# Kernel tuning notes

Hardware: AMD Instinct MI355X
Metric: run time of the kernel (lower is better)

## Reference

```python
import jax, jax.numpy as jnp
import numpy as np

B, S, IN, H = 64, 512, 64, 512


def _lin_init(key, fan_in, fan_out):
    k1, k2 = jax.random.split(key)
    bound = 1.0 / np.sqrt(fan_in)
    W = jax.random.uniform(k1, (fan_in, fan_out), jnp.float32, -bound, bound)
    b = jax.random.uniform(k2, (fan_out,), jnp.float32, -bound, bound)
    return W, b


def setup_inputs() -> dict:
    key = jax.random.key(0)
    ks = jax.random.split(key, 5)
    x = jax.random.normal(ks[0], (B, S, IN), jnp.float32)
    # Layer 0: 5 gates fused -> [IN+H, 5H]; layer 1 -> [H+H, 5H]
    W0, b0 = _lin_init(ks[1], IN + H, 5 * H)
    W1, b1 = _lin_init(ks[2], H + H, 5 * H)
    Wa, ba = _lin_init(ks[3], H, 1)
    Wfc, bfc = _lin_init(ks[4], H, 1)
    return {"x": x, "W0": W0, "b0": b0, "W1": W1, "b1": b1,
            "Wa": Wa, "ba": ba, "Wfc": Wfc, "bfc": bfc}


def _cell(xt, h, c, W, b):
    # one fused GEMM for the 5 gates (same math as 5 separate Linears)
    g = jnp.concatenate([xt, h], axis=-1) @ W + b  # [B, 5H]
    f, i, ch, o, e = jnp.split(g, 5, axis=-1)
    f = jax.nn.sigmoid(f)
    i = jax.nn.sigmoid(i)
    ch = jnp.tanh(ch)
    o = jax.nn.sigmoid(o)
    e = jax.nn.sigmoid(e)
    c_new = f * c + i * ch
    h_lin = o * jnp.tanh(c_new)
    h_new = e * jnp.exp(h_lin) + (1.0 - e) * h_lin  # exponential gating
    return h_new, c_new


def reference(x, W0, b0, W1, b1, Wa, ba, Wfc, bfc):
    Bx = x.shape[0]
    z = jnp.zeros((Bx, H), x.dtype)

    def step(carry, xt):
        (h0, c0), (h1, c1) = carry
        h0, c0 = _cell(xt, h0, c0, W0, b0)
        h1, c1 = _cell(h0, h1, c1, W1, b1)
        return ((h0, c0), (h1, c1)), h1

    _, hs = jax.lax.scan(step, ((z, z), (z, z)), jnp.swapaxes(x, 0, 1))
    lstm_out = jnp.swapaxes(hs, 0, 1)  # [B, S, H]
    att = jax.nn.softmax(lstm_out @ Wa + ba, axis=1)  # [B, S, 1], softmax over seq
    ctx = jnp.sum(att * lstm_out, axis=1)  # [B, H]
    out = ctx @ Wfc + bfc  # [B, 1]
    return out, att
```

## Files before the change

### kernel.cpp

```cpp
#include <hip/hip_runtime.h>
#include <hip/hip_cooperative_groups.h>
#include <math.h>

namespace cg = cooperative_groups;

#define BB 64
#define SS 512
#define INF 64
#define HH 512
#define G5 2560

typedef unsigned short u16;
typedef __attribute__((ext_vector_type(8))) short short8v;
typedef __attribute__((ext_vector_type(4))) float f32x4;

__global__ void init_kernel(float* __restrict__ p, int n) {
    int i = blockIdx.x * blockDim.x + threadIdx.x;
    if (i < n) p[i] = 0.f;
}

__device__ __forceinline__ void bf16_split(float f, u16& hi, u16& lo) {
    unsigned u = __float_as_uint(f);
    unsigned h = (u + 0x7FFFu + ((u >> 16) & 1u)) >> 16;
    float fh = __uint_as_float(h << 16);
    float r = f - fh;
    unsigned ur = __float_as_uint(r);
    unsigned l = (ur + 0x7FFFu + ((ur >> 16) & 1u)) >> 16;
    hi = (u16)h; lo = (u16)l;
}

__device__ __forceinline__ short8v ldfrag(const u16* p, int lane) {
    return *(const short8v*)(p + ((size_t)lane << 3));
}

__device__ __forceinline__ short8v llc_load(const u16* p, int lane) {
    short8v r;
    const u16* addr = p + ((size_t)lane << 3);
    asm volatile("global_load_dwordx4 %0, %1, off sc0 sc1"
                 : "=v"(r) : "v"(addr) : "memory");
    return r;
}

__global__ __launch_bounds__(256) void wrepack_frag(
    const float* __restrict__ W, u16* __restrict__ wf, int NS)
{
    const int s = blockIdx.x, J = blockIdx.y;
    const int tid = threadIdx.x;
    for (int v = tid; v < 2560; v += 256) {
        int g = v >> 9, rem = v & 511, kloc = rem >> 4, jloc = rem & 15;
        float w = W[(size_t)(s * 32 + kloc) * G5 + g * 512 + J * 16 + jloc];
        u16 hi, lo; bf16_split(w, hi, lo);
        int l = ((kloc >> 3) << 4) | jloc;
        size_t base = ((((size_t)J * 5 + g) * NS + s) * 2) * 512;
        size_t off = (size_t)l * 8 + (kloc & 7);
        wf[base + off] = hi;
        wf[base + 512 + off] = lo;
    }
}

__global__ __launch_bounds__(256) void xfrag_kernel(
    const float* __restrict__ x, u16* __restrict__ xf)
{
    const int t = blockIdx.x, tid = threadIdx.x;
    const size_t tb = (size_t)t * 2 * 4096;
    for (int rep = 0; rep < 4; ++rep) {
        int rrow = (tid >> 4) + rep * 16;
        int kq = (tid & 15) * 4;
        float4 v = *(const float4*)(x + ((size_t)rrow * SS + t) * INF + kq);
        float vals[4] = {v.x, v.y, v.z, v.w};
        #pragma unroll
        for (int c = 0; c < 4; ++c) {
            int k = kq + c;
            int sloc = k >> 5, kloc = k & 31;
            int m = rrow >> 4, rowloc = rrow & 15;
            int l = rowloc | ((kloc >> 3) << 4);
            size_t off = (size_t)sloc * 2048 + m * 512 + l * 8 + (kloc & 7);
            u16 hi, lo; bf16_split(vals[c], hi, lo);
            xf[tb + off] = hi;
            xf[tb + 4096 + off] = lo;
        }
    }
}

__device__ __forceinline__ void dom_arrive(unsigned* bar, int dom, int step) {
    unsigned r = __hip_atomic_fetch_add(bar + dom * 32, 1u,
                                        __ATOMIC_RELAXED, __HIP_MEMORY_SCOPE_AGENT);
    if (r == (unsigned)(step + 1) * 32u - 1u)
        __hip_atomic_store(bar + dom * 32 + 16, (unsigned)(step + 1),
                           __ATOMIC_RELAXED, __HIP_MEMORY_SCOPE_AGENT);
}
__device__ __forceinline__ void dom_wait(unsigned* bar, int dom, int val) {
    while ((int)__hip_atomic_load(bar + dom * 32 + 16,
                                  __ATOMIC_RELAXED, __HIP_MEMORY_SCOPE_AGENT) < val) {}
}

template<bool ISL1>
__device__ __forceinline__ void run_layer(
    const u16* __restrict__ xf, const u16* __restrict__ wf,
    u16* __restrict__ h0f, u16* __restrict__ h1f,
    const float* __restrict__ bv, float* __restrict__ lstm_out,
    unsigned* __restrict__ bar, float (*red)[5][64][4])
{
    constexpr int NS   = ISL1 ? 32 : 18;
    constexpr int MAXK = ISL1 ? 4 : 3;

    const int tid  = threadIdx.x;
    const int lane = tid & 63;
    const int wv   = tid >> 6;
    const int blk  = (int)blockIdx.x & 127;
    const int qq = blk >> 3, rr = blk & 7;
    const int J = rr * 4 + (qq & 3);
    const int m = qq >> 2;
    const int domSelf  = (ISL1 ? 4 : 0) + m;
    const int domOther = (ISL1 ? 0 : 4) + m;

    const int rowloc = (tid & 255) >> 4, jloc = tid & 15;
    const int row = m * 16 + rowloc;
    const int jg  = J * 16 + jloc;
    const int ltid = ((rowloc >> 2) << 4) | jloc;
    const int itid = rowloc & 3;

    float bias[5];
    #pragma unroll
    for (int g = 0; g < 5; ++g) bias[g] = bv[g * HH + jg];

    const int wkloc = ((J & 1) << 4) | jloc;
    const int wof = ((J >> 1) * 4 + m) * 512
                  + (rowloc | ((wkloc >> 3) << 4)) * 8 + (jloc & 7);

    short8v wH[MAXK][5], wL[MAXK][5];
    #pragma unroll
    for (int i = 0; i < MAXK; ++i) {
        const int s = wv + 8 * i;
        if (s < NS) {
            #pragma unroll
            for (int g = 0; g < 5; ++g) {
                const u16* wb = wf + ((((size_t)J * 5 + g) * NS + s) * 2) * 512;
                wH[i][g] = ldfrag(wb, lane);
                wL[i][g] = ldfrag(wb + 512, lane);
            }
        }
    }

    float c_reg = 0.f;
    float pend  = 0.f;

    for (int w = 0; w < SS; ++w) {
        if (tid == 0) {
            if (ISL1) {
                if (w >= 1) dom_wait(bar, domSelf, w);
                dom_wait(bar, domOther, w + 1);
            } else {
                if (w >= 1) dom_wait(bar, domSelf, w);
                if (w >= 4) dom_wait(bar, domOther, w - 3);
            }
        }
        __syncthreads();

        if (ISL1 && w >= 1 && tid < 256)
            lstm_out[((size_t)row * SS + (w - 1)) * HH + jg] = pend;

        short8v aH[MAXK], aL[MAXK];
        #pragma unroll
        for (int i = 0; i < MAXK; ++i) {
            const int s = wv + 8 * i;
            if (s < NS) {
                if (ISL1) {
                    const u16* p0;
                    const u16* p1;
                    if (s < 16) {
                        p0 = h0f + (size_t)((((w & 3) * 2 + 0) * 32768) + s * 2048 + m * 512);
                        p1 = h0f + (size_t)((((w & 3) * 2 + 1) * 32768) + s * 2048 + m * 512);
                    } else {
                        p0 = h1f + (size_t)(((((w + 1) & 1) * 2 + 0) * 32768) + (s - 16) * 2048 + m * 512);
                        p1 = h1f + (size_t)(((((w + 1) & 1) * 2 + 1) * 32768) + (s - 16) * 2048 + m * 512);
                    }
                    aH[i] = llc_load(p0, lane); aL[i] = llc_load(p1, lane);
                } else {
                    if (s < 2) {
                        const u16* p0 = xf + (size_t)((w * 2 + 0) * 4096 + s * 2048 + m * 512);
                        const u16* p1 = xf + (size_t)((w * 2 + 1) * 4096 + s * 2048 + m * 512);
                        aH[i] = ldfrag(p0, lane); aL[i] = ldfrag(p1, lane);
                    } else {
                        const u16* p0 = h0f + (size_t)(((((w + 3) & 3) * 2 + 0) * 32768) + (s - 2) * 2048 + m * 512);
                        const u16* p1 = h0f + (size_t)(((((w + 3) & 3) * 2 + 1) * 32768) + (s - 2) * 2048 + m * 512);
                        aH[i] = llc_load(p0, lane); aL[i] = llc_load(p1, lane);
                    }
                }
            }
        }

        asm volatile("s_waitcnt vmcnt(0)" ::: "memory");
        __builtin_amdgcn_sched_barrier(0);

        f32x4 acc[5];
        #pragma unroll
        for (int g = 0; g < 5; ++g) acc[g] = (f32x4){0.f, 0.f, 0.f, 0.f};

        #pragma unroll
        for (int i = 0; i < MAXK; ++i) {
            const int s = wv + 8 * i;
            if (s < NS) {
                #pragma unroll
                for (int g = 0; g < 5; ++g) {
                    acc[g] = __builtin_amdgcn_mfma_f32_16x16x32_bf16(aH[i], wH[i][g], acc[g], 0, 0, 0);
                    acc[g] = __builtin_amdgcn_mfma_f32_16x16x32_bf16(aH[i], wL[i][g], acc[g], 0, 0, 0);
                    acc[g] = __builtin_amdgcn_mfma_f32_16x16x32_bf16(aL[i], wH[i][g], acc[g], 0, 0, 0);
                }
            }
        }

        #pragma unroll
        for (int g = 0; g < 5; ++g)
            *(f32x4*)&red[wv][g][lane][0] = acc[g];
        __syncthreads();

        if (tid < 256) {
            float gv[5];
            #pragma unroll
            for (int g = 0; g < 5; ++g)
                gv[g] = ((red[0][g][ltid][itid] + red[1][g][ltid][itid])
                      +  (red[2][g][ltid][itid] + red[3][g][ltid][itid]))
                      + ((red[4][g][ltid][itid] + red[5][g][ltid][itid])
                      +  (red[6][g][ltid][itid] + red[7][g][ltid][itid]))
                      + bias[g];

            float f  = 1.f / (1.f + expf(-gv[0]));
            float i_ = 1.f / (1.f + expf(-gv[1]));
            float ch = tanhf(gv[2]);
            float o  = 1.f / (1.f + expf(-gv[3]));
            float e_ = 1.f / (1.f + expf(-gv[4]));

            c_reg = f * c_reg + i_ * ch;
            float hl = o * tanhf(c_reg);
            float hn = e_ * expf(hl) + (1.f - e_) * hl;

            u16 hi, lo; bf16_split(hn, hi, lo);
            if (ISL1) {
                const int par = w & 1;
                __hip_atomic_store(h1f + (size_t)((par * 2 + 0) * 32768) + wof, hi,
                                   __ATOMIC_RELAXED, __HIP_MEMORY_SCOPE_AGENT);
                __hip_atomic_store(h1f + (size_t)((par * 2 + 1) * 32768) + wof, lo,
                                   __ATOMIC_RELAXED, __HIP_MEMORY_SCOPE_AGENT);
                pend = hn;
            } else {
                const int par = w & 3;
                __hip_atomic_store(h0f + (size_t)((par * 2 + 0) * 32768) + wof, hi,
                                   __ATOMIC_RELAXED, __HIP_MEMORY_SCOPE_AGENT);
                __hip_atomic_store(h0f + (size_t)((par * 2 + 1) * 32768) + wof, lo,
                                   __ATOMIC_RELAXED, __HIP_MEMORY_SCOPE_AGENT);
            }
        }
        __syncthreads();
        if (tid == 0) dom_arrive(bar, domSelf, w);
    }
    if (ISL1 && threadIdx.x < 256)
        lstm_out[((size_t)row * SS + (SS - 1)) * HH + jg] = pend;
}

__global__ __launch_bounds__(512, 1) void persist_mfma(
    const u16* __restrict__ xf,
    const u16* __restrict__ wf0, const u16* __restrict__ wf1,
    const float* __restrict__ b0v, const float* __restrict__ b1v,
    u16* __restrict__ h0f, u16* __restrict__ h1f,
    float* __restrict__ lstm_out, unsigned* __restrict__ bar)
{
    __shared__ float red[8][5][64][4];
    if (blockIdx.x >= 128)
        run_layer<true >(xf, wf1, h0f, h1f, b1v, lstm_out, bar, red);
    else
        run_layer<false>(xf, wf0, h0f, h1f, b0v, lstm_out, bar, red);
}

__global__ __launch_bounds__(256) void repack_kernel(
    const float* __restrict__ W, float* __restrict__ P, int K)
{
    __shared__ float tile[64][65];
    const int tid = threadIdx.x;
    const int kt = blockIdx.x;
    const int c0 = blockIdx.y * 64;

    for (int e = tid; e < 64 * 16; e += 256) {
        int kr = e >> 4, cq = (e & 15) * 4;
        float4 v = *(const float4*)(W + (size_t)(kt * 64 + kr) * G5 + c0 + cq);
        tile[kr][cq + 0] = v.x; tile[kr][cq + 1] = v.y;
        tile[kr][cq + 2] = v.z; tile[kr][cq + 3] = v.w;
    }
    __syncthreads();

    const int gate = c0 >> 9;
    const int jb   = c0 & 511;
    for (int e = tid; e < 64 * 16; e += 256) {
        int lr = e >> 4;
        int kq = (e & 15) * 4;
        int j  = jb + lr;
        int g  = j >> 1;
        int c  = j & 1;
        int orow = g * 10 + gate * 2 + c;
        float4 v;
        v.x = tile[kq + 0][lr]; v.y = tile[kq + 1][lr];
        v.z = tile[kq + 2][lr]; v.w = tile[kq + 3][lr];
        *(float4*)(P + (size_t)orow * K + kt * 64 + kq) = v;
    }
}

__global__ __launch_bounds__(256) void xpose_kernel(
    const float* __restrict__ x, float* __restrict__ xT)
{
    __shared__ float tile[64][68];
    const int tid = threadIdx.x;
    const int t = blockIdx.x;

    for (int e = tid; e < 64 * 16; e += 256) {
        int row = e >> 4, kq = (e & 15) * 4;
        float4 v = *(const float4*)(x + ((size_t)row * SS + t) * INF + kq);
        tile[row][kq + 0] = v.x; tile[row][kq + 1] = v.y;
        tile[row][kq + 2] = v.z; tile[row][kq + 3] = v.w;
    }
    __syncthreads();
    float* dst = xT + (size_t)t * (INF * BB);
    for (int e = tid; e < INF * BB; e += 256) {
        int k = e >> 6, r = e & 63;
        dst[(k >> 2) * 256 + r * 4 + (k & 3)] = tile[r][k];
    }
}

__device__ __forceinline__ void gemm_seg(
    const float4* __restrict__ ap, const float4* __restrict__ wq,
    int K4, int nq, float* __restrict__ acc)
{
    #pragma unroll 2
    for (int q = 0; q < nq; ++q) {
        float4 a  = ap[q * 64];
        float4 w0 = wq[q + 0 * K4];
        float4 w1 = wq[q + 1 * K4];
        float4 w2 = wq[q + 2 * K4];
        float4 w3 = wq[q + 3 * K4];
        float4 w4 = wq[q + 4 * K4];
        float4 w5 = wq[q + 5 * K4];
        float4 w6 = wq[q + 6 * K4];
        float4 w7 = wq[q + 7 * K4];
        float4 w8 = wq[q + 8 * K4];
        float4 w9 = wq[q + 9 * K4];
        acc[0]=fmaf(a.x,w0.x,acc[0]); acc[0]=fmaf(a.y,w0.y,acc[0]);
        acc[0]=fmaf(a.z,w0.z,acc[0]); acc[0]=fmaf(a.w,w0.w,acc[0]);
        acc[1]=fmaf(a.x,w1.x,acc[1]); acc[1]=fmaf(a.y,w1.y,acc[1]);
        acc[1]=fmaf(a.z,w1.z,acc[1]); acc[1]=fmaf(a.w,w1.w,acc[1]);
        acc[2]=fmaf(a.x,w2.x,acc[2]); acc[2]=fmaf(a.y,w2.y,acc[2]);
        acc[2]=fmaf(a.z,w2.z,acc[2]); acc[2]=fmaf(a.w,w2.w,acc[2]);
        acc[3]=fmaf(a.x,w3.x,acc[3]); acc[3]=fmaf(a.y,w3.y,acc[3]);
        acc[3]=fmaf(a.z,w3.z,acc[3]); acc[3]=fmaf(a.w,w3.w,acc[3]);
        acc[4]=fmaf(a.x,w4.x,acc[4]); acc[4]=fmaf(a.y,w4.y,acc[4]);
        acc[4]=fmaf(a.z,w4.z,acc[4]); acc[4]=fmaf(a.w,w4.w,acc[4]);
        acc[5]=fmaf(a.x,w5.x,acc[5]); acc[5]=fmaf(a.y,w5.y,acc[5]);
        acc[5]=fmaf(a.z,w5.z,acc[5]); acc[5]=fmaf(a.w,w5.w,acc[5]);
        acc[6]=fmaf(a.x,w6.x,acc[6]); acc[6]=fmaf(a.y,w6.y,acc[6]);
        acc[6]=fmaf(a.z,w6.z,acc[6]); acc[6]=fmaf(a.w,w6.w,acc[6]);
        acc[7]=fmaf(a.x,w7.x,acc[7]); acc[7]=fmaf(a.y,w7.y,acc[7]);
        acc[7]=fmaf(a.z,w7.z,acc[7]); acc[7]=fmaf(a.w,w7.w,acc[7]);
        acc[8]=fmaf(a.x,w8.x,acc[8]); acc[8]=fmaf(a.y,w8.y,acc[8]);
        acc[8]=fmaf(a.z,w8.z,acc[8]); acc[8]=fmaf(a.w,w8.w,acc[8]);
        acc[9]=fmaf(a.x,w9.x,acc[9]); acc[9]=fmaf(a.y,w9.y,acc[9]);
        acc[9]=fmaf(a.z,w9.z,acc[9]); acc[9]=fmaf(a.w,w9.w,acc[9]);
    }
}

__global__ __launch_bounds__(256, 2) void step512_kernel(
    const float* __restrict__ xT,
    const float* __restrict__ P0, const float* __restrict__ b0v,
    const float* __restrict__ P1, const float* __restrict__ b1v,
    float* __restrict__ h0buf, float* __restrict__ h1buf,
    float* __restrict__ c0buf, float* __restrict__ c1buf,
    float* __restrict__ lstm_out, int t)
{
    __shared__ float W_s[10 * 1024];
    __shared__ float red[4][10][64];

    const int tid  = threadIdx.x;
    const int lane = tid & 63;
    const int wv   = tid >> 6;
    const bool isL1 = (blockIdx.x >= 256);
    const int blk  = (int)blockIdx.x & 255;
    const int g    = (blk & 7) * 32 + (blk >> 3);
    const int j    = g * 2 + (wv & 1);

    const bool active = isL1 ? (t >= 1) : (t < SS);
    if (!active) return;

    const int K  = isL1 ? 1024 : 576;
    const int K4 = K >> 2;
    const int QK = K >> 2;
    const int k0 = wv * QK;

    {
        const float* Pg = (isL1 ? P1 : P0) + (size_t)g * 10 * K;
        const int n4 = 10 * K / 4;
        for (int i = tid; i < n4; i += 256)
            *(float4*)&W_s[i * 4] = *(const float4*)(Pg + (size_t)i * 4);
    }
    __syncthreads();

    const int tm1 = t - 1;
    const float* h0prev = h0buf + ((t + 1) & 1) * (BB * HH);
    const float* h0cur  = h0buf + (tm1 & 1) * (BB * HH);
    const float* h1prev = h1buf + ((tm1 + 1) & 1) * (BB * HH);

    const float4* wq0 = (const float4*)W_s + (k0 >> 2);

    float acc[10];
    #pragma unroll
    for (int r = 0; r < 10; ++r) acc[r] = 0.f;

    if (!isL1) {
        if (wv == 0) {
            const float4* aX = (const float4*)(xT + (size_t)t * (INF * BB)) + lane;
            const float4* aH = (const float4*)h0prev + lane;
            gemm_seg(aX, wq0,      K4, 16, acc);
            gemm_seg(aH, wq0 + 16, K4, 20, acc);
        } else {
            const float4* aH = (const float4*)h0prev + (36 * wv - 16) * 64 + lane;
            gemm_seg(aH, wq0, K4, 36, acc);
        }
    } else {
        const float* src = (wv < 2) ? h0cur : h1prev;
        const float4* aH = (const float4*)src + (wv & 2 ? (wv - 2) : wv) * 4096 + lane;
        gemm_seg(aH, wq0, K4, 64, acc);
    }

    #pragma unroll
    for (int r = 0; r < 10; ++r) red[wv][r][lane] = acc[r];
    __syncthreads();

    if (wv < 2) {
        const float* bv = isL1 ? b1v : b0v;
        float gv[5];
        #pragma unroll
        for (int gate = 0; gate < 5; ++gate) {
            int r = gate * 2 + wv;
            gv[gate] = red[0][r][lane] + red[1][r][lane]
                     + red[2][r][lane] + red[3][r][lane] + bv[gate * HH + j];
        }
        float f  = 1.f / (1.f + expf(-gv[0]));
        float i_ = 1.f / (1.f + expf(-gv[1]));
        float ch = tanhf(gv[2]);
        float o  = 1.f / (1.f + expf(-gv[3]));
        float e_ = 1.f / (1.f + expf(-gv[4]));

        float* cb = (isL1 ? c1buf : c0buf) + j * BB + lane;
        float c = f * (*cb) + i_ * ch;
        *cb = c;
        float hl = o * tanhf(c);
        float hn = e_ * expf(hl) + (1.f - e_) * hl;

        const int hoff = (j >> 2) * 256 + lane * 4 + (j & 3);
        if (!isL1) {
            h0buf[(t & 1) * (BB * HH) + hoff] = hn;
        } else {
            h1buf[(tm1 & 1) * (BB * HH) + hoff] = hn;
            lstm_out[((size_t)lane * SS + tm1) * HH + j] = hn;
        }
    }
}

__global__ __launch_bounds__(256) void attn_kernel(
    const float* __restrict__ lstm_out,
    const float* __restrict__ Wa, const float* __restrict__ ba,
    const float* __restrict__ Wfc, const float* __restrict__ bfc,
    float* __restrict__ dout)
{
    const int b = blockIdx.x;
    const int tid = threadIdx.x;
    const int lane = tid & 63;
    const int wave = tid >> 6;

    __shared__ float wa_s[HH];
    __shared__ float logit[SS];
    __shared__ float wred[4];

    for (int ii = tid; ii < HH; ii += 256) wa_s[ii] = Wa[ii];
    __syncthreads();

    const float* Lb = lstm_out + (size_t)b * SS * HH;

    for (int tt = wave; tt < SS; tt += 4) {
        const float* rowp = Lb + (size_t)tt * HH;
        float s = 0.f;
        for (int jc = lane; jc < HH; jc += 64) s += rowp[jc] * wa_s[jc];
        #pragma unroll
        for (int off = 32; off > 0; off >>= 1) s += __shfl_down(s, off, 64);
        if (lane == 0) logit[tt] = s + ba[0];
    }
    __syncthreads();

    float m = -1e30f;
    for (int ii = tid; ii < SS; ii += 256) m = fmaxf(m, logit[ii]);
    #pragma unroll
    for (int off = 32; off > 0; off >>= 1) m = fmaxf(m, __shfl_down(m, off, 64));
    if (lane == 0) wred[wave] = m;
    __syncthreads();
    m = fmaxf(fmaxf(wred[0], wred[1]), fmaxf(wred[2], wred[3]));
    __syncthreads();

    float ssum = 0.f;
    for (int ii = tid; ii < SS; ii += 256) {
        float e = expf(logit[ii] - m);
        logit[ii] = e;
        ssum += e;
    }
    #pragma unroll
    for (int off = 32; off > 0; off >>= 1) ssum += __shfl_down(ssum, off, 64);
    if (lane == 0) wred[wave] = ssum;
    __syncthreads();
    ssum = wred[0] + wred[1] + wred[2] + wred[3];
    float inv = 1.f / ssum;
    __syncthreads();

    for (int ii = tid; ii < SS; ii += 256) {
        float a = logit[ii] * inv;
        logit[ii] = a;
        dout[BB + (size_t)b * SS + ii] = a;
    }
    __syncthreads();

    float ctx0 = 0.f, ctx1 = 0.f;
    for (int tt = 0; tt < SS; ++tt) {
        float a = logit[tt];
        ctx0 += a * Lb[(size_t)tt * HH + tid];
        ctx1 += a * Lb[(size_t)tt * HH + tid + 256];
    }

    float p = ctx0 * Wfc[tid] + ctx1 * Wfc[tid + 256];
    #pragma unroll
    for (int off = 32; off > 0; off >>= 1) p += __shfl_down(p, off, 64);
    __syncthreads();
    if (lane == 0) wred[wave] = p;
    __syncthreads();
    if (tid == 0) dout[b] = wred[0] + wred[1] + wred[2] + wred[3] + bfc[0];
}

extern "C" void kernel_launch(void* const* d_in, const int* in_sizes, int n_in,
                              void* d_out, int out_size, void* d_ws, size_t ws_size,
                              hipStream_t stream) {
    const float* x   = (const float*)d_in[0];
    const float* W0  = (const float*)d_in[1];
    const float* b0  = (const float*)d_in[2];
    const float* W1  = (const float*)d_in[3];
    const float* b1  = (const float*)d_in[4];
    const float* Wa  = (const float*)d_in[5];
    const float* ba  = (const float*)d_in[6];
    const float* Wfc = (const float*)d_in[7];
    const float* bfc = (const float*)d_in[8];
    float* out = (float*)d_out;
    float* ws  = (float*)d_ws;

    float* h0q  = ws;
    float* h1q  = h0q + 2 * BB * HH;
    float* c0   = h1q + 2 * BB * HH;
    float* c1   = c0 + BB * HH;
    u16*   h0f  = (u16*)(c1 + BB * HH);
    u16*   h1f  = h0f + 262144;
    unsigned* bar = (unsigned*)(h1f + 131072);
    float* lstm = (float*)(bar + 1024);
    float* WA   = lstm + (size_t)BB * SS * HH;
    float* WB   = WA + (size_t)G5 * (INF + HH);
    float* XF   = WB + (size_t)G5 * (HH + HH);
    u16* wf0 = (u16*)WA;
    u16* wf1 = (u16*)WB;
    u16* xf  = (u16*)XF;

    const int n_init = 6 * BB * HH + 262144 / 2 + 131072 / 2 + 1024;
    init_kernel<<<(n_init + 255) / 256, 256, 0, stream>>>(ws, n_init);

    wrepack_frag<<<dim3(18, 32), 256, 0, stream>>>(W0, wf0, 18);
    wrepack_frag<<<dim3(32, 32), 256, 0, stream>>>(W1, wf1, 32);
    xfrag_kernel<<<SS, 256, 0, stream>>>(x, xf);

    void* args[] = { (void*)&xf, (void*)&wf0, (void*)&wf1, (void*)&b0, (void*)&b1,
                     (void*)&h0f, (void*)&h1f, (void*)&lstm, (void*)&bar };
    hipError_t cerr = hipLaunchCooperativeKernel((void*)persist_mfma,
                                                 dim3(256), dim3(512),
                                                 args, 0, stream);
    if (cerr != hipSuccess) {
        repack_kernel<<<dim3((INF + HH) / 64, 40), 256, 0, stream>>>(W0, WA, INF + HH);
        repack_kernel<<<dim3((HH + HH) / 64, 40), 256, 0, stream>>>(W1, WB, HH + HH);
        xpose_kernel<<<SS, 256, 0, stream>>>(x, XF);
        for (int t = 0; t <= SS; ++t) {
            step512_kernel<<<512, 256, 0, stream>>>(XF, WA, b0, WB, b1,
                                                    h0q, h1q, c0, c1, lstm, t);
        }
    }

    attn_kernel<<<BB, 256, 0, stream>>>(lstm, Wa, ba, Wfc, bfc, out);
}
```

Baseline: 2.122 ms.

## Replace block barrier with per-thread domain waits and split loads around waits

Drops the tid==0 wait followed by __syncthreads at the top of each timestep. Every thread now spins on the domain flags itself, and the loads are split into two phases. Inputs gated by the other layer's barrier (or x, which needs no barrier) are loaded first, then the thread waits on its own domain and loads the self-dependent hidden state. The aim is to remove the block-wide sync and overlap part of the operand fetch with the self-domain wait. The cost is that all threads poll the atomic flags, which raises memory traffic.

Result: slower. 3.479 ms (+63.9%).

```diff
diff --git a/kernel.cpp b/kernel.cpp
--- a/kernel.cpp
+++ b/kernel.cpp
@@ -89,7 +89,7 @@
         __hip_atomic_store(bar + dom * 32 + 16, (unsigned)(step + 1),
                            __ATOMIC_RELAXED, __HIP_MEMORY_SCOPE_AGENT);
 }
-__device__ __forceinline__ void dom_wait(unsigned* bar, int dom, int val) {
+__device__ __forceinline__ void dom_wait_all(unsigned* bar, int dom, int val) {
     while ((int)__hip_atomic_load(bar + dom * 32 + 16,
                                   __ATOMIC_RELAXED, __HIP_MEMORY_SCOPE_AGENT) < val) {}
 }
@@ -146,46 +146,46 @@
     float pend  = 0.f;
 
     for (int w = 0; w < SS; ++w) {
-        if (tid == 0) {
-            if (ISL1) {
-                if (w >= 1) dom_wait(bar, domSelf, w);
-                dom_wait(bar, domOther, w + 1);
-            } else {
-                if (w >= 1) dom_wait(bar, domSelf, w);
-                if (w >= 4) dom_wait(bar, domOther, w - 3);
-            }
-        }
-        __syncthreads();
-
-        if (ISL1 && w >= 1 && tid < 256)
-            lstm_out[((size_t)row * SS + (w - 1)) * HH + jg] = pend;
-
         short8v aH[MAXK], aL[MAXK];
-        #pragma unroll
-        for (int i = 0; i < MAXK; ++i) {
-            const int s = wv + 8 * i;
-            if (s < NS) {
-                if (ISL1) {
-                    const u16* p0;
-                    const u16* p1;
-                    if (s < 16) {
-                        p0 = h0f + (size_t)((((w & 3) * 2 + 0) * 32768) + s * 2048 + m * 512);
-                        p1 = h0f + (size_t)((((w & 3) * 2 + 1) * 32768) + s * 2048 + m * 512);
-                    } else {
-                        p0 = h1f + (size_t)(((((w + 1) & 1) * 2 + 0) * 32768) + (s - 16) * 2048 + m * 512);
-                        p1 = h1f + (size_t)(((((w + 1) & 1) * 2 + 1) * 32768) + (s - 16) * 2048 + m * 512);
-                    }
+
+        if (ISL1) {
+            dom_wait_all(bar, domOther, w + 1);
+            #pragma unroll
+            for (int i = 0; i < 2; ++i) {
+                const int s = wv + 8 * i;
+                const u16* p0 = h0f + (size_t)((((w & 3) * 2 + 0) * 32768) + s * 2048 + m * 512);
+                const u16* p1 = h0f + (size_t)((((w & 3) * 2 + 1) * 32768) + s * 2048 + m * 512);
+                aH[i] = llc_load(p0, lane); aL[i] = llc_load(p1, lane);
+            }
+            if (w >= 1 && tid < 256)
+                lstm_out[((size_t)row * SS + (w - 1)) * HH + jg] = pend;
+        } else {
+            if (w >= 4) dom_wait_all(bar, domOther, w - 3);
+            if (wv < 2) {
+                const u16* p0 = xf + (size_t)((w * 2 + 0) * 4096 + wv * 2048 + m * 512);
+                const u16* p1 = xf + (size_t)((w * 2 + 1) * 4096 + wv * 2048 + m * 512);
+                aH[0] = ldfrag(p0, lane); aL[0] = ldfrag(p1, lane);
+            }
+        }
+
+        if (w >= 1) dom_wait_all(bar, domSelf, w);
+
+        if (ISL1) {
+            #pragma unroll
+            for (int i = 2; i < 4; ++i) {
+                const int s = wv + 8 * i - 16;
+                const u16* p0 = h1f + (size_t)(((((w + 1) & 1) * 2 + 0) * 32768) + s * 2048 + m * 512);
+                const u16* p1 = h1f + (size_t)(((((w + 1) & 1) * 2 + 1) * 32768) + s * 2048 + m * 512);
+                aH[i] = llc_load(p0, lane); aL[i] = llc_load(p1, lane);
+            }
+        } else {
+            #pragma unroll
+            for (int i = 0; i < MAXK; ++i) {
+                const int s = wv + 8 * i;
+                if (s >= 2 && s < NS) {
+                    const u16* p0 = h0f + (size_t)(((((w + 3) & 3) * 2 + 0) * 32768) + (s - 2) * 2048 + m * 512);
+                    const u16* p1 = h0f + (size_t)(((((w + 3) & 3) * 2 + 1) * 32768) + (s - 2) * 2048 + m * 512);
                     aH[i] = llc_load(p0, lane); aL[i] = llc_load(p1, lane);
-                } else {
-                    if (s < 2) {
-                        const u16* p0 = xf + (size_t)((w * 2 + 0) * 4096 + s * 2048 + m * 512);
-                        const u16* p1 = xf + (size_t)((w * 2 + 1) * 4096 + s * 2048 + m * 512);
-                        aH[i] = ldfrag(p0, lane); aL[i] = ldfrag(p1, lane);
-                    } else {
-                        const u16* p0 = h0f + (size_t)(((((w + 3) & 3) * 2 + 0) * 32768) + (s - 2) * 2048 + m * 512);
-                        const u16* p1 = h0f + (size_t)(((((w + 3) & 3) * 2 + 1) * 32768) + (s - 2) * 2048 + m * 512);
-                        aH[i] = llc_load(p0, lane); aL[i] = llc_load(p1, lane);
-                    }
                 }
             }
         }
```
